# Kernel optimization log

Hardware: AMD Instinct MI355X
Metric: run time of the kernel (lower is better)

The kernel has to match this reference:

```python
import jax, jax.numpy as jnp
import numpy as np

B, D, K, S = 8192, 1024, 8192, 64  # batch, feature_dim, num_blocks, block_size
EPS = 1e-5


def layer_norm(x, g, b):
    mu = jnp.mean(x, axis=-1, keepdims=True)
    var = jnp.var(x, axis=-1, keepdims=True)
    return (x - mu) * jax.lax.rsqrt(var + EPS) * g + b


def setup_inputs() -> dict:
    key = jax.random.key(0)
    ks = jax.random.split(key, 12)
    s = 0.02
    return {
        "features": jax.random.normal(ks[0], (B, D), dtype=jnp.float32),
        "codebook": jax.random.normal(ks[1], (K, S), dtype=jnp.float32) * 0.1,
        # projection: Linear(D, 2S) -> ReLU -> LayerNorm(2S) -> Linear(2S, S)
        "proj_w1": jax.random.normal(ks[2], (D, 2 * S), dtype=jnp.float32) * s,
        "proj_b1": jnp.zeros((2 * S,), dtype=jnp.float32),
        "ln1_g": jnp.ones((2 * S,), dtype=jnp.float32),
        "ln1_b": jnp.zeros((2 * S,), dtype=jnp.float32),
        "proj_w2": jax.random.normal(ks[3], (2 * S, S), dtype=jnp.float32) * s,
        "proj_b2": jnp.zeros((S,), dtype=jnp.float32),
        # reconstruction: Linear(S, 2D) -> ReLU -> LayerNorm(2D) -> Linear(2D, D)
        "rec_w1": jax.random.normal(ks[4], (S, 2 * D), dtype=jnp.float32) * s,
        "rec_b1": jnp.zeros((2 * D,), dtype=jnp.float32),
        "ln2_g": jnp.ones((2 * D,), dtype=jnp.float32),
        "ln2_b": jnp.zeros((2 * D,), dtype=jnp.float32),
        "rec_w2": jax.random.normal(ks[5], (2 * D, D), dtype=jnp.float32) * s,
        "rec_b2": jnp.zeros((D,), dtype=jnp.float32),
    }


def reference(features, codebook, proj_w1, proj_b1, ln1_g, ln1_b, proj_w2, proj_b2,
              rec_w1, rec_b1, ln2_g, ln2_b, rec_w2, rec_b2):
    # --- encode ---
    h = jax.nn.relu(features @ proj_w1 + proj_b1)
    h = layer_norm(h, ln1_g, ln1_b)
    z = h @ proj_w2 + proj_b2  # [B, S] (dropout inactive in eval)
    # squared Euclidean distances; argmin identical to cdist(p=2) argmin
    d2 = (jnp.sum(z * z, axis=1, keepdims=True)
          - 2.0 * (z @ codebook.T)
          + jnp.sum(codebook * codebook, axis=1))  # [B, K]
    indices = jnp.argmin(d2, axis=1)  # [B]
    # usage scatter-add (buffer update in the torch module)
    block_usage = jnp.zeros((K,), dtype=jnp.float32).at[indices].add(1.0)
    # --- decode ---
    sel = codebook[indices]  # [B, S] embedding gather
    r = jax.nn.relu(sel @ rec_w1 + rec_b1)
    r = layer_norm(r, ln2_g, ln2_b)
    reconstructed = r @ rec_w2 + rec_b2  # [B, D]
    return reconstructed, indices, block_usage
```

## Files before the change

kernel.cpp:

```cpp
#include <hip/hip_runtime.h>
#include <hip/hip_bf16.h>
#include <stdint.h>

#define LN_EPS 1e-5f

typedef float f32x4 __attribute__((ext_vector_type(4)));
typedef short short8 __attribute__((ext_vector_type(8)));

__device__ __forceinline__ float bf2f(unsigned int u) {
  union { unsigned int i; float f; } x; x.i = u << 16; return x.f;
}
__device__ __forceinline__ unsigned short f2bf(float f) {
  unsigned int x = __float_as_uint(f);
  x += 0x7fffu + ((x >> 16) & 1u);
  return (unsigned short)(x >> 16);
}

__device__ __forceinline__ void gload16(const void* g, void* l) {
  __builtin_amdgcn_global_load_lds((const __attribute__((address_space(1))) unsigned int*)g,
                                   (__attribute__((address_space(3))) unsigned int*)l, 16, 0, 0);
}

__device__ __forceinline__ void stage_tile(const unsigned short* g, int ldg,
                                           unsigned short* lds, int wave, int lane) {
#pragma unroll
  for (int i = 0; i < 4; i++) {
    const int chunk = i * 4 + wave;
    const unsigned short* ga = g + (size_t)(chunk * 8 + (lane >> 3)) * ldg + (lane & 7) * 8;
    gload16(ga, lds + chunk * 512);
  }
}

__global__ __launch_bounds__(256) void k0_c2_zero(const float* __restrict__ CB,
                                                  float* __restrict__ C2,
                                                  float* __restrict__ usage) {
  const int g = blockIdx.x * 256 + threadIdx.x;
  const int code = g >> 4, l16 = g & 15;
  const float4 v = *(const float4*)&CB[(size_t)code * 64 + (l16 << 2)];
  float s = v.x * v.x + v.y * v.y + v.z * v.z + v.w * v.w;
#pragma unroll
  for (int m = 8; m >= 1; m >>= 1) s += __shfl_xor(s, m, 16);
  if (l16 == 0) C2[code] = s;
  if (g < 8192) usage[g] = 0.f;
}

__global__ __launch_bounds__(256) void k1_encode(const float* __restrict__ X,
                                                 const float* __restrict__ W1,
                                                 const float* __restrict__ B1,
                                                 const float* __restrict__ G1,
                                                 const float* __restrict__ Bn1,
                                                 const float* __restrict__ W2,
                                                 const float* __restrict__ B2,
                                                 float* __restrict__ Z) {
  __shared__ float At[64][20];
  __shared__ float Wc[64][128];
  __shared__ float Ht[128][20];
  const int t = threadIdx.x;
  const int row0 = blockIdx.x << 4;
  const int rg = t >> 6;
  const int r0 = rg << 2;
  const int cg = t & 63;
  const int c0 = cg << 1;
  const int lr = t >> 4, lkc = (t & 15) << 2;
  float acc[4][2] = {{0,0},{0,0},{0,0},{0,0}};

  for (int k0 = 0; k0 < 1024; k0 += 64) {
    __syncthreads();
    {
      const float4 av = *(const float4*)&X[(size_t)(row0 + lr) * 1024 + k0 + lkc];
      At[lkc + 0][lr] = av.x; At[lkc + 1][lr] = av.y;
      At[lkc + 2][lr] = av.z; At[lkc + 3][lr] = av.w;
    }
    {
      const float4* wsrc = (const float4*)&W1[(size_t)k0 * 128];
      float4* wdst = (float4*)&Wc[0][0];
#pragma unroll
      for (int i = 0; i < 8; i++) wdst[t + (i << 8)] = wsrc[t + (i << 8)];
    }
    __syncthreads();
#pragma unroll
    for (int kk = 0; kk < 64; kk++) {
      const float4 a = *(const float4*)&At[kk][r0];
      const float2 w = *(const float2*)&Wc[kk][c0];
      acc[0][0] = fmaf(a.x, w.x, acc[0][0]); acc[0][1] = fmaf(a.x, w.y, acc[0][1]);
      acc[1][0] = fmaf(a.y, w.x, acc[1][0]); acc[1][1] = fmaf(a.y, w.y, acc[1][1]);
      acc[2][0] = fmaf(a.z, w.x, acc[2][0]); acc[2][1] = fmaf(a.z, w.y, acc[2][1]);
      acc[3][0] = fmaf(a.w, w.x, acc[3][0]); acc[3][1] = fmaf(a.w, w.y, acc[3][1]);
    }
  }
  const float b1a = B1[c0], b1b = B1[c0 + 1];
  float h[4][2], s1[4], s2[4];
#pragma unroll
  for (int i = 0; i < 4; i++) {
    h[i][0] = fmaxf(acc[i][0] + b1a, 0.f);
    h[i][1] = fmaxf(acc[i][1] + b1b, 0.f);
    s1[i] = h[i][0] + h[i][1];
    s2[i] = h[i][0] * h[i][0] + h[i][1] * h[i][1];
  }
#pragma unroll
  for (int m = 32; m >= 1; m >>= 1) {
#pragma unroll
    for (int i = 0; i < 4; i++) { s1[i] += __shfl_xor(s1[i], m); s2[i] += __shfl_xor(s2[i], m); }
  }
  const float ga = G1[c0], gb = G1[c0 + 1], ba = Bn1[c0], bb = Bn1[c0 + 1];
#pragma unroll
  for (int i = 0; i < 4; i++) {
    const float mean = s1[i] * (1.f / 128.f);
    const float var  = s2[i] * (1.f / 128.f) - mean * mean;
    const float rs = rsqrtf(var + LN_EPS);
    Ht[c0 + 0][r0 + i] = (h[i][0] - mean) * rs * ga + ba;
    Ht[c0 + 1][r0 + i] = (h[i][1] - mean) * rs * gb + bb;
  }
  __syncthreads();
  float za[4] = {0, 0, 0, 0};
  for (int k = 0; k < 128; k++) {
    const float4 hv = *(const float4*)&Ht[k][r0];
    const float wv = W2[(k << 6) + cg];
    za[0] = fmaf(hv.x, wv, za[0]); za[1] = fmaf(hv.y, wv, za[1]);
    za[2] = fmaf(hv.z, wv, za[2]); za[3] = fmaf(hv.w, wv, za[3]);
  }
  const float b2v = B2[cg];
#pragma unroll
  for (int i = 0; i < 4; i++)
    Z[(size_t)(row0 + r0 + i) * 64 + cg] = za[i] + b2v;
}

__global__ __launch_bounds__(256) void k2_dist(const float* __restrict__ Z,
                                               const float* __restrict__ CB,
                                               const float* __restrict__ C2,
                                               float* __restrict__ Pval,
                                               int* __restrict__ Pidx) {
  __shared__ float Zt[64][34];
  __shared__ float Ct[64][130];
  const int t = threadIdx.x;
  const int lane = t & 63, wave = t >> 6;
  const int rowblk = blockIdx.x >> 2, quarter = blockIdx.x & 3;
  const int row0 = rowblk << 5;
  const int code0 = quarter << 11;
  const int r0 = (t >> 5) << 2;
  const int c0 = (lane & 31) << 2;

#pragma unroll
  for (int i = 0; i < 2; i++) {
    const int f = t + (i << 8);
    const int r = f >> 4, kc = (f & 15) << 2;
    const float4 v = *(const float4*)&Z[(size_t)(row0 + r) * 64 + kc];
    Zt[kc + 0][r] = v.x; Zt[kc + 1][r] = v.y;
    Zt[kc + 2][r] = v.z; Zt[kc + 3][r] = v.w;
  }

  const int wq = (wave << 4) + (lane >> 2);
  const int kb = (lane & 3) << 2;
  float4 st[8];
#define K2_PF(cr, r) \
  st[(cr) * 4 + (r)] = *(const float4*)&CB[(size_t)(code0 + chunk * 128 + (cr) * 64 + wq) * 64 + kb + 16 * (r)];
#define K2_WR(cr, r) { \
    const float4 v = st[(cr) * 4 + (r)]; \
    const int k2r = kb + 16 * (r); const int col = (cr) * 64 + wq; \
    Ct[k2r + 0][col] = v.x; Ct[k2r + 1][col] = v.y; \
    Ct[k2r + 2][col] = v.z; Ct[k2r + 3][col] = v.w; }

  {
    const int chunk = 0;
    K2_PF(0, 0) K2_PF(0, 1) K2_PF(0, 2) K2_PF(0, 3)
    K2_PF(1, 0) K2_PF(1, 1) K2_PF(1, 2) K2_PF(1, 3)
  }
  __syncthreads();

  float minv[4] = {3.4e38f, 3.4e38f, 3.4e38f, 3.4e38f};
  int   mini[4] = {0, 0, 0, 0};

  for (int c = 0; c < 16; c++) {
    K2_WR(0, 0) K2_WR(0, 1) K2_WR(0, 2) K2_WR(0, 3)
    K2_WR(1, 0) K2_WR(1, 1) K2_WR(1, 2) K2_WR(1, 3)
    __syncthreads();
    if (c + 1 < 16) {
      const int chunk = c + 1;
      K2_PF(0, 0) K2_PF(0, 1) K2_PF(0, 2) K2_PF(0, 3)
      K2_PF(1, 0) K2_PF(1, 1) K2_PF(1, 2) K2_PF(1, 3)
    }
    float acc[4][4];
#pragma unroll
    for (int i = 0; i < 4; i++)
#pragma unroll
      for (int j = 0; j < 4; j++) acc[i][j] = 0.f;
#pragma unroll 4
    for (int k = 0; k < 64; k++) {
      const float4 zv = *(const float4*)&Zt[k][r0];
      const float4 cv = *(const float4*)&Ct[k][c0];
      acc[0][0] = fmaf(zv.x, cv.x, acc[0][0]); acc[0][1] = fmaf(zv.x, cv.y, acc[0][1]);
      acc[0][2] = fmaf(zv.x, cv.z, acc[0][2]); acc[0][3] = fmaf(zv.x, cv.w, acc[0][3]);
      acc[1][0] = fmaf(zv.y, cv.x, acc[1][0]); acc[1][1] = fmaf(zv.y, cv.y, acc[1][1]);
      acc[1][2] = fmaf(zv.y, cv.z, acc[1][2]); acc[1][3] = fmaf(zv.y, cv.w, acc[1][3]);
      acc[2][0] = fmaf(zv.z, cv.x, acc[2][0]); acc[2][1] = fmaf(zv.z, cv.y, acc[2][1]);
      acc[2][2] = fmaf(zv.z, cv.z, acc[2][2]); acc[2][3] = fmaf(zv.z, cv.w, acc[2][3]);
      acc[3][0] = fmaf(zv.w, cv.x, acc[3][0]); acc[3][1] = fmaf(zv.w, cv.y, acc[3][1]);
      acc[3][2] = fmaf(zv.w, cv.z, acc[3][2]); acc[3][3] = fmaf(zv.w, cv.w, acc[3][3]);
    }
    const int codeb = code0 + (c << 7) + c0;
    const float4 c2v = *(const float4*)&C2[codeb];
    const float c2a[4] = {c2v.x, c2v.y, c2v.z, c2v.w};
#pragma unroll
    for (int i = 0; i < 4; i++)
#pragma unroll
      for (int j = 0; j < 4; j++) {
        const float s = fmaf(-2.f, acc[i][j], c2a[j]);
        if (s < minv[i]) { minv[i] = s; mini[i] = codeb + j; }
      }
    __syncthreads();
  }
#undef K2_PF
#undef K2_WR
#pragma unroll
  for (int m = 16; m >= 1; m >>= 1) {
#pragma unroll
    for (int i = 0; i < 4; i++) {
      const float ov = __shfl_xor(minv[i], m);
      const int   oi = __shfl_xor(mini[i], m);
      if (ov < minv[i] || (ov == minv[i] && oi < mini[i])) { minv[i] = ov; mini[i] = oi; }
    }
  }
  if ((lane & 31) == 0) {
#pragma unroll
    for (int i = 0; i < 4; i++) {
      const int r = row0 + r0 + i;
      Pval[r * 4 + quarter] = minv[i];
      Pidx[r * 4 + quarter] = mini[i];
    }
  }
}

__global__ __launch_bounds__(256) void k2_merge(const float* __restrict__ Pval,
                                                const int* __restrict__ Pidx,
                                                int* __restrict__ IDX,
                                                float* __restrict__ outIdx,
                                                float* __restrict__ usage) {
  const int r = blockIdx.x * 256 + threadIdx.x;
  const float4 v = *(const float4*)&Pval[r * 4];
  const int4   i = *(const int4*)&Pidx[r * 4];
  float bv = v.x; int bi = i.x;
  if (v.y < bv) { bv = v.y; bi = i.y; }
  if (v.z < bv) { bv = v.z; bi = i.z; }
  if (v.w < bv) { bv = v.w; bi = i.w; }
  IDX[r] = bi;
  outIdx[r] = (float)bi;
  atomicAdd(&usage[bi], 1.0f);
}

__global__ __launch_bounds__(256) void k_tcast(const float* __restrict__ src,
                                               unsigned short* __restrict__ dst,
                                               int R, int C) {
  __shared__ float T[32][33];
  const int tilesC = C >> 5;
  const int bx = blockIdx.x;
  const int tr = bx / tilesC, tc = bx - tr * tilesC;
  const int t = threadIdx.x;
  {
    const int r = t >> 3, c4 = (t & 7) << 2;
    const float4 v = *(const float4*)&src[(size_t)(tr * 32 + r) * C + tc * 32 + c4];
    T[r][c4] = v.x; T[r][c4 + 1] = v.y; T[r][c4 + 2] = v.z; T[r][c4 + 3] = v.w;
  }
  __syncthreads();
  const int c = t >> 3, r4 = (t & 7) << 2;
  ushort4 o;
  o.x = f2bf(T[r4 + 0][c]); o.y = f2bf(T[r4 + 1][c]);
  o.z = f2bf(T[r4 + 2][c]); o.w = f2bf(T[r4 + 3][c]);
  *(ushort4*)&dst[(size_t)(tc * 32 + c) * R + tr * 32 + r4] = o;
}

__global__ __launch_bounds__(256) void k3_gather(const float* __restrict__ CB,
                                                 const int* __restrict__ IDX,
                                                 unsigned short* __restrict__ SEL) {
  const int g = blockIdx.x * 256 + threadIdx.x;
  const int row = g >> 4, c4 = (g & 15) << 2;
  const int code = IDX[row];
  const float4 v = *(const float4*)&CB[(size_t)code * 64 + c4];
  ushort4 o;
  o.x = f2bf(v.x); o.y = f2bf(v.y); o.z = f2bf(v.z); o.w = f2bf(v.w);
  *(ushort4*)&SEL[(size_t)row * 64 + c4] = o;
}

__global__ __launch_bounds__(256) void k4_rec1(const unsigned short* __restrict__ A,
                                               const unsigned short* __restrict__ Bt,
                                               const float* __restrict__ bias,
                                               unsigned short* __restrict__ H) {
  __shared__ __align__(16) unsigned short As[128 * 64];
  __shared__ __align__(16) unsigned short Bs[128 * 64];
  const int t = threadIdx.x;
  const int wave = t >> 6, lane = t & 63;
  const int bx = blockIdx.x;
  const int tm = bx >> 4, tn = bx & 15;
  const int m0 = tm << 7, n0 = tn << 7;
  const int wm = wave >> 1, wn = wave & 1;
  const int ln15 = lane & 15, lk = (lane >> 4) << 3;
  stage_tile(A + (size_t)m0 * 64, 64, As, wave, lane);
  stage_tile(Bt + (size_t)n0 * 64, 64, Bs, wave, lane);
  asm volatile("s_waitcnt vmcnt(0)" ::: "memory");
  __syncthreads();
  f32x4 acc[4][4];
#pragma unroll
  for (int i = 0; i < 4; i++)
#pragma unroll
    for (int j = 0; j < 4; j++) acc[i][j] = (f32x4){0.f, 0.f, 0.f, 0.f};
#pragma unroll
  for (int ks = 0; ks < 2; ks++) {
    short8 a[4], b[4];
#pragma unroll
    for (int i = 0; i < 4; i++)
      a[i] = *(const short8*)&As[(wm * 64 + i * 16 + ln15) * 64 + ks * 32 + lk];
#pragma unroll
    for (int j = 0; j < 4; j++)
      b[j] = *(const short8*)&Bs[(wn * 64 + j * 16 + ln15) * 64 + ks * 32 + lk];
#pragma unroll
    for (int i = 0; i < 4; i++)
#pragma unroll
      for (int j = 0; j < 4; j++)
        acc[i][j] = __builtin_amdgcn_mfma_f32_16x16x32_bf16(a[i], b[j], acc[i][j], 0, 0, 0);
  }
  const int l4 = (lane >> 4) << 2;
#pragma unroll
  for (int j = 0; j < 4; j++) {
    const int col = n0 + wn * 64 + j * 16 + ln15;
    const float bv = bias[col];
#pragma unroll
    for (int i = 0; i < 4; i++) {
      const int row = m0 + wm * 64 + i * 16 + l4;
#pragma unroll
      for (int r = 0; r < 4; r++)
        H[(size_t)(row + r) * 2048 + col] = f2bf(fmaxf(acc[i][j][r] + bv, 0.f));
    }
  }
}

__global__ __launch_bounds__(256) void k5_ln(unsigned short* __restrict__ H,
                                             const float* __restrict__ G,
                                             const float* __restrict__ B) {
  const int row = blockIdx.x, t = threadIdx.x;
  unsigned short* p = H + (size_t)row * 2048 + t * 8;
  const uint4 raw = *(const uint4*)p;
  float v[8];
  v[0] = bf2f(raw.x & 0xffffu); v[1] = bf2f(raw.x >> 16);
  v[2] = bf2f(raw.y & 0xffffu); v[3] = bf2f(raw.y >> 16);
  v[4] = bf2f(raw.z & 0xffffu); v[5] = bf2f(raw.z >> 16);
  v[6] = bf2f(raw.w & 0xffffu); v[7] = bf2f(raw.w >> 16);
  float s1 = 0.f, s2 = 0.f;
#pragma unroll
  for (int i = 0; i < 8; i++) { s1 += v[i]; s2 = fmaf(v[i], v[i], s2); }
#pragma unroll
  for (int m = 32; m >= 1; m >>= 1) { s1 += __shfl_xor(s1, m); s2 += __shfl_xor(s2, m); }
  __shared__ float red[8];
  const int lane = t & 63, wv = t >> 6;
  if (lane == 0) { red[wv] = s1; red[4 + wv] = s2; }
  __syncthreads();
  s1 = red[0] + red[1] + red[2] + red[3];
  s2 = red[4] + red[5] + red[6] + red[7];
  const float mean = s1 * (1.f / 2048.f);
  const float var  = s2 * (1.f / 2048.f) - mean * mean;
  const float rs = rsqrtf(var + LN_EPS);
  const int c = t * 8;
  unsigned int w0, w1, w2, w3;
  {
    const float o0 = (v[0] - mean) * rs * G[c + 0] + B[c + 0];
    const float o1 = (v[1] - mean) * rs * G[c + 1] + B[c + 1];
    w0 = (unsigned int)f2bf(o0) | ((unsigned int)f2bf(o1) << 16);
  }
  {
    const float o0 = (v[2] - mean) * rs * G[c + 2] + B[c + 2];
    const float o1 = (v[3] - mean) * rs * G[c + 3] + B[c + 3];
    w1 = (unsigned int)f2bf(o0) | ((unsigned int)f2bf(o1) << 16);
  }
  {
    const float o0 = (v[4] - mean) * rs * G[c + 4] + B[c + 4];
    const float o1 = (v[5] - mean) * rs * G[c + 5] + B[c + 5];
    w2 = (unsigned int)f2bf(o0) | ((unsigned int)f2bf(o1) << 16);
  }
  {
    const float o0 = (v[6] - mean) * rs * G[c + 6] + B[c + 6];
    const float o1 = (v[7] - mean) * rs * G[c + 7] + B[c + 7];
    w3 = (unsigned int)f2bf(o0) | ((unsigned int)f2bf(o1) << 16);
  }
  uint4 outw; outw.x = w0; outw.y = w1; outw.z = w2; outw.w = w3;
  *(uint4*)p = outw;
}

__global__ __launch_bounds__(256) void k6_rec2(const unsigned short* __restrict__ A,
                                               const unsigned short* __restrict__ Bt,
                                               const float* __restrict__ bias,
                                               float* __restrict__ C) {
  __shared__ __align__(16) unsigned short As[2][128 * 64];
  __shared__ __align__(16) unsigned short Bs[2][128 * 64];
  const int t = threadIdx.x;
  const int wave = t >> 6, lane = t & 63;
  const int bx = blockIdx.x;
  const int tm = bx >> 3, tn = bx & 7;
  const int m0 = tm << 7, n0 = tn << 7;
  const int wm = wave >> 1, wn = wave & 1;
  const int ln15 = lane & 15, lk = (lane >> 4) << 3;
  f32x4 acc[4][4];
#pragma unroll
  for (int i = 0; i < 4; i++)
#pragma unroll
    for (int j = 0; j < 4; j++) acc[i][j] = (f32x4){0.f, 0.f, 0.f, 0.f};

  stage_tile(A + (size_t)m0 * 2048, 2048, As[0], wave, lane);
  stage_tile(Bt + (size_t)n0 * 2048, 2048, Bs[0], wave, lane);
  asm volatile("s_waitcnt vmcnt(0)" ::: "memory");
  __syncthreads();

  int cur = 0;
  for (int kt = 0; kt < 32; kt++) {
    if (kt + 1 < 32) {
      const int k0 = (kt + 1) << 6;
      stage_tile(A + (size_t)m0 * 2048 + k0, 2048, As[cur ^ 1], wave, lane);
      stage_tile(Bt + (size_t)n0 * 2048 + k0, 2048, Bs[cur ^ 1], wave, lane);
    }
#pragma unroll
    for (int ks = 0; ks < 2; ks++) {
      short8 a[4], b[4];
#pragma unroll
      for (int i = 0; i < 4; i++)
        a[i] = *(const short8*)&As[cur][(wm * 64 + i * 16 + ln15) * 64 + ks * 32 + lk];
#pragma unroll
      for (int j = 0; j < 4; j++)
        b[j] = *(const short8*)&Bs[cur][(wn * 64 + j * 16 + ln15) * 64 + ks * 32 + lk];
#pragma unroll
      for (int i = 0; i < 4; i++)
#pragma unroll
        for (int j = 0; j < 4; j++)
          acc[i][j] = __builtin_amdgcn_mfma_f32_16x16x32_bf16(a[i], b[j], acc[i][j], 0, 0, 0);
    }
    asm volatile("s_waitcnt vmcnt(0)" ::: "memory");
    __syncthreads();
    cur ^= 1;
  }
  const int l4 = (lane >> 4) << 2;
#pragma unroll
  for (int j = 0; j < 4; j++) {
    const int col = n0 + wn * 64 + j * 16 + ln15;
    const float bv = bias[col];
#pragma unroll
    for (int i = 0; i < 4; i++) {
      const int row = m0 + wm * 64 + i * 16 + l4;
#pragma unroll
      for (int r = 0; r < 4; r++)
        C[(size_t)(row + r) * 1024 + col] = acc[i][j][r] + bv;
    }
  }
}

extern "C" void kernel_launch(void* const* d_in, const int* in_sizes, int n_in,
                              void* d_out, int out_size, void* d_ws, size_t ws_size,
                              hipStream_t stream) {
  (void)in_sizes; (void)n_in; (void)out_size; (void)ws_size;
  const float* features = (const float*)d_in[0];
  const float* codebook = (const float*)d_in[1];
  const float* proj_w1  = (const float*)d_in[2];
  const float* proj_b1  = (const float*)d_in[3];
  const float* ln1_g    = (const float*)d_in[4];
  const float* ln1_b    = (const float*)d_in[5];
  const float* proj_w2  = (const float*)d_in[6];
  const float* proj_b2  = (const float*)d_in[7];
  const float* rec_w1   = (const float*)d_in[8];
  const float* rec_b1   = (const float*)d_in[9];
  const float* ln2_g    = (const float*)d_in[10];
  const float* ln2_b    = (const float*)d_in[11];
  const float* rec_w2   = (const float*)d_in[12];
  const float* rec_b2   = (const float*)d_in[13];

  float* out_recon = (float*)d_out;
  float* out_idx   = out_recon + (size_t)8192 * 1024;
  float* out_usage = out_idx + 8192;

  char* ws = (char*)d_ws;
  float*          c2  = (float*)(ws);
  int*            idx = (int*)(ws + 32768);
  float*          z   = (float*)(ws + 65536);
  unsigned short* sel = (unsigned short*)(ws + 2162688);
  unsigned short* w1t = (unsigned short*)(ws + 3211264);
  unsigned short* w2t = (unsigned short*)(ws + 3473408);
  unsigned short* h1  = (unsigned short*)(ws + 7667712);
  float* pval = (float*)(ws + 2162688);
  int*   pidx = (int*)(ws + 2162688 + 131072);

  k0_c2_zero<<<512, 256, 0, stream>>>(codebook, c2, out_usage);
  k1_encode <<<512, 256, 0, stream>>>(features, proj_w1, proj_b1, ln1_g, ln1_b,
                                      proj_w2, proj_b2, z);
  k2_dist   <<<1024, 256, 0, stream>>>(z, codebook, c2, pval, pidx);
  k2_merge  <<<32, 256, 0, stream>>>(pval, pidx, idx, out_idx, out_usage);
  k_tcast   <<<128, 256, 0, stream>>>(rec_w1, w1t, 64, 2048);
  k_tcast   <<<2048, 256, 0, stream>>>(rec_w2, w2t, 2048, 1024);
  k3_gather <<<512, 256, 0, stream>>>(codebook, idx, sel);
  k4_rec1   <<<1024, 256, 0, stream>>>(sel, w1t, rec_b1, h1);
  k5_ln     <<<8192, 256, 0, stream>>>(h1, ln2_g, ln2_b);
  k6_rec2   <<<512, 256, 0, stream>>>(h1, w2t, rec_b2, out_recon);
}
```

Before: 427.5 us.

## Enlarge distance-kernel row tile and single-buffer the rec2 GEMM staging

The distance kernel now handles 64 rows per block instead of 32, giving each thread 8x4 accumulators. Each codebook tile loaded into shared memory is reused across twice as many rows, and half as many blocks are launched. Separately, the rec2 GEMM drops double buffering for a single shared buffer with sync, load, wait, sync each k-step. This frees shared memory, which may raise occupancy, but global loads no longer overlap with MFMA work. The larger register footprint in k2_dist may lower its occupancy.

Result: faster. 379.0 us (-11.3%).

```diff
diff --git a/kernel.cpp b/kernel.cpp
--- a/kernel.cpp
+++ b/kernel.cpp
@@ -130,18 +130,18 @@
                                                const float* __restrict__ C2,
                                                float* __restrict__ Pval,
                                                int* __restrict__ Pidx) {
-  __shared__ float Zt[64][34];
-  __shared__ float Ct[64][130];
+  __shared__ float Zt[64][68];
+  __shared__ float Ct[64][132];
   const int t = threadIdx.x;
   const int lane = t & 63, wave = t >> 6;
   const int rowblk = blockIdx.x >> 2, quarter = blockIdx.x & 3;
-  const int row0 = rowblk << 5;
+  const int row0 = rowblk << 6;
   const int code0 = quarter << 11;
-  const int r0 = (t >> 5) << 2;
+  const int r0 = (t >> 5) << 3;
   const int c0 = (lane & 31) << 2;
 
 #pragma unroll
-  for (int i = 0; i < 2; i++) {
+  for (int i = 0; i < 4; i++) {
     const int f = t + (i << 8);
     const int r = f >> 4, kc = (f & 15) << 2;
     const float4 v = *(const float4*)&Z[(size_t)(row0 + r) * 64 + kc];
@@ -167,8 +167,10 @@
   }
   __syncthreads();
 
-  float minv[4] = {3.4e38f, 3.4e38f, 3.4e38f, 3.4e38f};
-  int   mini[4] = {0, 0, 0, 0};
+  float minv[8];
+  int   mini[8];
+#pragma unroll
+  for (int i = 0; i < 8; i++) { minv[i] = 3.4e38f; mini[i] = 0; }
 
   for (int c = 0; c < 16; c++) {
     K2_WR(0, 0) K2_WR(0, 1) K2_WR(0, 2) K2_WR(0, 3)
@@ -179,29 +181,29 @@
       K2_PF(0, 0) K2_PF(0, 1) K2_PF(0, 2) K2_PF(0, 3)
       K2_PF(1, 0) K2_PF(1, 1) K2_PF(1, 2) K2_PF(1, 3)
     }
-    float acc[4][4];
-#pragma unroll
-    for (int i = 0; i < 4; i++)
+    float acc[8][4];
+#pragma unroll
+    for (int i = 0; i < 8; i++)
 #pragma unroll
       for (int j = 0; j < 4; j++) acc[i][j] = 0.f;
-#pragma unroll 4
+#pragma unroll 2
     for (int k = 0; k < 64; k++) {
-      const float4 zv = *(const float4*)&Zt[k][r0];
+      const float4 za = *(const float4*)&Zt[k][r0];
+      const float4 zb = *(const float4*)&Zt[k][r0 + 4];
       const float4 cv = *(const float4*)&Ct[k][c0];
-      acc[0][0] = fmaf(zv.x, cv.x, acc[0][0]); acc[0][1] = fmaf(zv.x, cv.y, acc[0][1]);
-      acc[0][2] = fmaf(zv.x, cv.z, acc[0][2]); acc[0][3] = fmaf(zv.x, cv.w, acc[0][3]);
-      acc[1][0] = fmaf(zv.y, cv.x, acc[1][0]); acc[1][1] = fmaf(zv.y, cv.y, acc[1][1]);
-      acc[1][2] = fmaf(zv.y, cv.z, acc[1][2]); acc[1][3] = fmaf(zv.y, cv.w, acc[1][3]);
-      acc[2][0] = fmaf(zv.z, cv.x, acc[2][0]); acc[2][1] = fmaf(zv.z, cv.y, acc[2][1]);
-      acc[2][2] = fmaf(zv.z, cv.z, acc[2][2]); acc[2][3] = fmaf(zv.z, cv.w, acc[2][3]);
-      acc[3][0] = fmaf(zv.w, cv.x, acc[3][0]); acc[3][1] = fmaf(zv.w, cv.y, acc[3][1]);
-      acc[3][2] = fmaf(zv.w, cv.z, acc[3][2]); acc[3][3] = fmaf(zv.w, cv.w, acc[3][3]);
+      const float zr[8] = {za.x, za.y, za.z, za.w, zb.x, zb.y, zb.z, zb.w};
+      const float cc[4] = {cv.x, cv.y, cv.z, cv.w};
+#pragma unroll
+      for (int i = 0; i < 8; i++)
+#pragma unroll
+        for (int j = 0; j < 4; j++)
+          acc[i][j] = fmaf(zr[i], cc[j], acc[i][j]);
     }
     const int codeb = code0 + (c << 7) + c0;
     const float4 c2v = *(const float4*)&C2[codeb];
     const float c2a[4] = {c2v.x, c2v.y, c2v.z, c2v.w};
 #pragma unroll
-    for (int i = 0; i < 4; i++)
+    for (int i = 0; i < 8; i++)
 #pragma unroll
       for (int j = 0; j < 4; j++) {
         const float s = fmaf(-2.f, acc[i][j], c2a[j]);
@@ -214,7 +216,7 @@
 #pragma unroll
   for (int m = 16; m >= 1; m >>= 1) {
 #pragma unroll
-    for (int i = 0; i < 4; i++) {
+    for (int i = 0; i < 8; i++) {
       const float ov = __shfl_xor(minv[i], m);
       const int   oi = __shfl_xor(mini[i], m);
       if (ov < minv[i] || (ov == minv[i] && oi < mini[i])) { minv[i] = ov; mini[i] = oi; }
@@ -222,7 +224,7 @@
   }
   if ((lane & 31) == 0) {
 #pragma unroll
-    for (int i = 0; i < 4; i++) {
+    for (int i = 0; i < 8; i++) {
       const int r = row0 + r0 + i;
       Pval[r * 4 + quarter] = minv[i];
       Pidx[r * 4 + quarter] = mini[i];
@@ -387,8 +389,8 @@
                                                const unsigned short* __restrict__ Bt,
                                                const float* __restrict__ bias,
                                                float* __restrict__ C) {
-  __shared__ __align__(16) unsigned short As[2][128 * 64];
-  __shared__ __align__(16) unsigned short Bs[2][128 * 64];
+  __shared__ __align__(16) unsigned short As[128 * 64];
+  __shared__ __align__(16) unsigned short Bs[128 * 64];
   const int t = threadIdx.x;
   const int wave = t >> 6, lane = t & 63;
   const int bx = blockIdx.x;
@@ -402,36 +404,27 @@
 #pragma unroll
     for (int j = 0; j < 4; j++) acc[i][j] = (f32x4){0.f, 0.f, 0.f, 0.f};
 
-  stage_tile(A + (size_t)m0 * 2048, 2048, As[0], wave, lane);
-  stage_tile(Bt + (size_t)n0 * 2048, 2048, Bs[0], wave, lane);
-  asm volatile("s_waitcnt vmcnt(0)" ::: "memory");
-  __syncthreads();
-
-  int cur = 0;
-  for (int kt = 0; kt < 32; kt++) {
-    if (kt + 1 < 32) {
-      const int k0 = (kt + 1) << 6;
-      stage_tile(A + (size_t)m0 * 2048 + k0, 2048, As[cur ^ 1], wave, lane);
-      stage_tile(Bt + (size_t)n0 * 2048 + k0, 2048, Bs[cur ^ 1], wave, lane);
-    }
+  for (int k0 = 0; k0 < 2048; k0 += 64) {
+    __syncthreads();
+    stage_tile(A + (size_t)m0 * 2048 + k0, 2048, As, wave, lane);
+    stage_tile(Bt + (size_t)n0 * 2048 + k0, 2048, Bs, wave, lane);
+    asm volatile("s_waitcnt vmcnt(0)" ::: "memory");
+    __syncthreads();
 #pragma unroll
     for (int ks = 0; ks < 2; ks++) {
       short8 a[4], b[4];
 #pragma unroll
       for (int i = 0; i < 4; i++)
-        a[i] = *(const short8*)&As[cur][(wm * 64 + i * 16 + ln15) * 64 + ks * 32 + lk];
+        a[i] = *(const short8*)&As[(wm * 64 + i * 16 + ln15) * 64 + ks * 32 + lk];
 #pragma unroll
       for (int j = 0; j < 4; j++)
-        b[j] = *(const short8*)&Bs[cur][(wn * 64 + j * 16 + ln15) * 64 + ks * 32 + lk];
+        b[j] = *(const short8*)&Bs[(wn * 64 + j * 16 + ln15) * 64 + ks * 32 + lk];
 #pragma unroll
       for (int i = 0; i < 4; i++)
 #pragma unroll
         for (int j = 0; j < 4; j++)
           acc[i][j] = __builtin_amdgcn_mfma_f32_16x16x32_bf16(a[i], b[j], acc[i][j], 0, 0, 0);
     }
-    asm volatile("s_waitcnt vmcnt(0)" ::: "memory");
-    __syncthreads();
-    cur ^= 1;
   }
   const int l4 = (lane >> 4) << 2;
 #pragma unroll
@@ -485,7 +478,7 @@
   k0_c2_zero<<<512, 256, 0, stream>>>(codebook, c2, out_usage);
   k1_encode <<<512, 256, 0, stream>>>(features, proj_w1, proj_b1, ln1_g, ln1_b,
                                       proj_w2, proj_b2, z);
-  k2_dist   <<<1024, 256, 0, stream>>>(z, codebook, c2, pval, pidx);
+  k2_dist   <<<512, 256, 0, stream>>>(z, codebook, c2, pval, pidx);
   k2_merge  <<<32, 256, 0, stream>>>(pval, pidx, idx, out_idx, out_usage);
   k_tcast   <<<128, 256, 0, stream>>>(rec_w1, w1t, 64, 2048);
   k_tcast   <<<2048, 256, 0, stream>>>(rec_w2, w2t, 2048, 1024);
```
